# Performance work log

Measured on AMD Instinct MI355X. Metric: run time of the kernel, lower is better.

Reference implementation:

```python
import jax, jax.numpy as jnp
import numpy as np


def setup_inputs() -> dict:
    key = jax.random.key(0)
    k1, k2 = jax.random.split(key)
    # [batch, seq, in_features] activations
    x = jax.random.normal(k1, (4, 4096, 2048), dtype=jnp.float32)
    # fp32 master weight [out_features, in_features]; quantized inside reference
    weight = jax.random.normal(k2, (2048, 2048), dtype=jnp.float32) * 0.02
    return {"x": x, "weight": weight}


def reference(x, weight):
    num_bits = 8
    Qn = -(2 ** (num_bits - 1))       # -128
    Qp = 2 ** (num_bits - 1) - 1      # 127

    # Per-row absmax int8 activation quantization (activation_quant)
    si = Qp / jnp.clip(jnp.max(jnp.abs(x), axis=-1, keepdims=True), 1e-5)  # [B,S,1]
    qx = jnp.clip(jnp.round(x * si), Qn, Qp)  # int8 values held in fp32 (exact)

    # Ternary weight quantization (weight_quant): sw scalar = 1/mean|W|
    sw = 1.0 / jnp.clip(jnp.mean(jnp.abs(weight)), 1e-5)
    qw = jnp.clip(jnp.round(weight * sw), -1.0, 1.0)  # {-1,0,1}

    acc = jnp.einsum("bsk,nk->bsn", qx, qw)  # [B,S,out]

    # post_quant_process: dequantize by si and sw, cast to half
    out = ((acc / si) / sw).astype(jnp.float16)
    return out
```

## Files before the change

### kernel.cpp

```cpp
#include <hip/hip_runtime.h>

#define K_DIM 2048
#define N_DIM 2048
#define M_DIM 16384

typedef int v4i __attribute__((ext_vector_type(4)));


__device__ __forceinline__ void lds16(const void* g, void* l) {
    __builtin_amdgcn_global_load_lds(
        (const __attribute__((address_space(1))) unsigned int*)g,
        (__attribute__((address_space(3))) unsigned int*)l,
        16, 0, 0);
}

__global__ __launch_bounds__(256) void k_wsum(const float* __restrict__ w,
                                              double* __restrict__ wsum) {
    int tid = blockIdx.x * 256 + threadIdx.x;
    int stride = gridDim.x * 256;
    const float4* w4 = (const float4*)w;
    double s = 0.0;
    for (int i = tid; i < (N_DIM * K_DIM / 4); i += stride) {
        float4 v = w4[i];
        s += (double)fabsf(v.x);
        s += (double)fabsf(v.y);
        s += (double)fabsf(v.z);
        s += (double)fabsf(v.w);
    }
#pragma unroll
    for (int off = 32; off; off >>= 1) s += __shfl_xor(s, off, 64);
    __shared__ double part[4];
    int lane = threadIdx.x & 63, wv = threadIdx.x >> 6;
    if (lane == 0) part[wv] = s;
    __syncthreads();
    if (threadIdx.x == 0) atomicAdd(wsum, part[0] + part[1] + part[2] + part[3]);
}

__global__ __launch_bounds__(256) void k_quant_w(const float* __restrict__ w,
                                                 signed char* __restrict__ qw,
                                                 const double* __restrict__ wsum,
                                                 float* __restrict__ invsw_out) {
    float mean = (float)(*wsum * (1.0 / (double)(N_DIM * K_DIM)));
    float meanc = fmaxf(mean, 1e-5f);
    float sw = 1.0f / meanc;
    int tid = blockIdx.x * 256 + threadIdx.x;
    float4 v = ((const float4*)w)[tid];
    int q0 = (int)fminf(fmaxf(rintf(v.x * sw), -1.f), 1.f);
    int q1 = (int)fminf(fmaxf(rintf(v.y * sw), -1.f), 1.f);
    int q2 = (int)fminf(fmaxf(rintf(v.z * sw), -1.f), 1.f);
    int q3 = (int)fminf(fmaxf(rintf(v.w * sw), -1.f), 1.f);
    ((int*)qw)[tid] = (q0 & 255) | ((q1 & 255) << 8) | ((q2 & 255) << 16) | ((q3 & 255) << 24);
    if (tid == 0) *invsw_out = meanc;
}

__global__ __launch_bounds__(256) void k_quant_x(const float* __restrict__ x,
                                                 signed char* __restrict__ qx,
                                                 float* __restrict__ si_out) {
    int row = blockIdx.x * 4 + (threadIdx.x >> 6);
    int lane = threadIdx.x & 63;
    const float4* xr = (const float4*)(x + (size_t)row * K_DIM);
    float4 v[8];
    float mx = 0.f;
#pragma unroll
    for (int c = 0; c < 8; c++) {
        v[c] = xr[c * 64 + lane];
        mx = fmaxf(mx, fmaxf(fmaxf(fabsf(v[c].x), fabsf(v[c].y)),
                             fmaxf(fabsf(v[c].z), fabsf(v[c].w))));
    }
#pragma unroll
    for (int off = 32; off; off >>= 1) mx = fmaxf(mx, __shfl_xor(mx, off, 64));
    float si = 127.0f / fmaxf(mx, 1e-5f);
    if (lane == 0) si_out[row] = si;
    int* qr = (int*)(qx + (size_t)row * K_DIM);
#pragma unroll
    for (int c = 0; c < 8; c++) {
        int q0 = (int)fminf(fmaxf(rintf(v[c].x * si), -128.f), 127.f);
        int q1 = (int)fminf(fmaxf(rintf(v[c].y * si), -128.f), 127.f);
        int q2 = (int)fminf(fmaxf(rintf(v[c].z * si), -128.f), 127.f);
        int q3 = (int)fminf(fmaxf(rintf(v[c].w * si), -128.f), 127.f);
        qr[c * 64 + lane] = (q0 & 255) | ((q1 & 255) << 8) | ((q2 & 255) << 16) | ((q3 & 255) << 24);
    }
}

__global__ __launch_bounds__(256) void k_gemm(const signed char* __restrict__ qx,
                                              const signed char* __restrict__ qw,
                                              const float* __restrict__ si,
                                              const float* __restrict__ invsw_p,
                                              float* __restrict__ out) {
    __shared__ __align__(16) signed char As[128 * 64];
    __shared__ __align__(16) signed char Bs[128 * 64];
    const int t = threadIdx.x;
    const int lane = t & 63, wv = t >> 6;
    const int wr = wv >> 1, wc = wv & 1;
    const int lr = lane & 15, lq = lane >> 4;
    const int bm = blockIdx.y, bn = blockIdx.x;

    const int sRow = t >> 2;
    const int sCol = (t & 3) << 4;
    const signed char* aB0 = qx + (size_t)(bm * 128 + sRow) * K_DIM + sCol;
    const signed char* aB1 = aB0 + (size_t)64 * K_DIM;
    const signed char* bB0 = qw + (size_t)(bn * 128 + sRow) * K_DIM + sCol;
    const signed char* bB1 = bB0 + (size_t)64 * K_DIM;
    const int t16 = t << 4;

    v4i acc[4][4] = {};

    for (int k0 = 0; k0 < K_DIM; k0 += 64) {
        lds16(aB0 + k0, (signed char*)As + t16);
        lds16(aB1 + k0, (signed char*)As + 4096 + t16);
        lds16(bB0 + k0, (signed char*)Bs + t16);
        lds16(bB1 + k0, (signed char*)Bs + 4096 + t16);
        __syncthreads();

        v4i af[4], bf[4];
#pragma unroll
        for (int mt = 0; mt < 4; mt++)
            af[mt] = *(const v4i*)(As + ((wr * 64 + mt * 16 + lr) * 64 + lq * 16));
#pragma unroll
        for (int nt = 0; nt < 4; nt++)
            bf[nt] = *(const v4i*)(Bs + ((wc * 64 + nt * 16 + lr) * 64 + lq * 16));
#pragma unroll
        for (int mt = 0; mt < 4; mt++)
#pragma unroll
            for (int nt = 0; nt < 4; nt++)
                acc[mt][nt] = __builtin_amdgcn_mfma_i32_16x16x64_i8(af[mt], bf[nt], acc[mt][nt], 0, 0, 0);
        __syncthreads();
    }

    float invsw = *invsw_p;
#pragma unroll
    for (int mt = 0; mt < 4; mt++) {
        int rowb = bm * 128 + wr * 64 + mt * 16 + lq * 4;
        float sc[4];
#pragma unroll
        for (int r = 0; r < 4; r++) sc[r] = invsw / si[rowb + r];
#pragma unroll
        for (int nt = 0; nt < 4; nt++) {
            int col = bn * 128 + wc * 64 + nt * 16 + lr;
#pragma unroll
            for (int r = 0; r < 4; r++) {
                float vv = (float)acc[mt][nt][r] * sc[r];
                out[(size_t)(rowb + r) * N_DIM + col] = (float)(_Float16)vv;
            }
        }
    }
}

extern "C" void kernel_launch(void* const* d_in, const int* in_sizes, int n_in,
                              void* d_out, int out_size, void* d_ws, size_t ws_size,
                              hipStream_t stream) {
    const float* x = (const float*)d_in[0];
    const float* w = (const float*)d_in[1];
    float* out = (float*)d_out;
    char* ws = (char*)d_ws;

    double* wsum = (double*)ws;
    float* invsw = (float*)(ws + 8);
    float* si = (float*)(ws + 256);
    signed char* qw = (signed char*)(ws + 256 + 65536);
    signed char* qx = qw + (size_t)N_DIM * K_DIM;

    hipMemsetAsync(wsum, 0, 8, stream);
    k_wsum<<<1024, 256, 0, stream>>>(w, wsum);
    k_quant_w<<<4096, 256, 0, stream>>>(w, qw, wsum, invsw);
    k_quant_x<<<4096, 256, 0, stream>>>(x, qx, si);
    k_gemm<<<dim3(N_DIM / 128, M_DIM / 128), 256, 0, stream>>>(qx, qw, si, invsw, out);
}
```

Before: 336.3 us.

## Use 32x32x32 int8 MFMA with 256x128 tiles and deterministic weight-sum reduction

```diff
diff --git a/kernel.cpp b/kernel.cpp
--- a/kernel.cpp
+++ b/kernel.cpp
@@ -5,6 +5,7 @@
 #define M_DIM 16384
 
 typedef int v4i __attribute__((ext_vector_type(4)));
+typedef int v16i __attribute__((ext_vector_type(16)));
 
 
 __device__ __forceinline__ void lds16(const void* g, void* l) {
@@ -15,7 +16,7 @@
 }
 
 __global__ __launch_bounds__(256) void k_wsum(const float* __restrict__ w,
-                                              double* __restrict__ wsum) {
+                                              double* __restrict__ part) {
     int tid = blockIdx.x * 256 + threadIdx.x;
     int stride = gridDim.x * 256;
     const float4* w4 = (const float4*)w;
@@ -29,20 +30,33 @@
     }
 #pragma unroll
     for (int off = 32; off; off >>= 1) s += __shfl_xor(s, off, 64);
-    __shared__ double part[4];
+    __shared__ double sp[4];
     int lane = threadIdx.x & 63, wv = threadIdx.x >> 6;
-    if (lane == 0) part[wv] = s;
+    if (lane == 0) sp[wv] = s;
     __syncthreads();
-    if (threadIdx.x == 0) atomicAdd(wsum, part[0] + part[1] + part[2] + part[3]);
+    if (threadIdx.x == 0) part[blockIdx.x] = sp[0] + sp[1] + sp[2] + sp[3];
+}
+
+__global__ __launch_bounds__(256) void k_wred(const double* __restrict__ part,
+                                              float* __restrict__ invsw_out) {
+    double s = part[threadIdx.x];
+#pragma unroll
+    for (int off = 32; off; off >>= 1) s += __shfl_xor(s, off, 64);
+    __shared__ double sp[4];
+    int lane = threadIdx.x & 63, wv = threadIdx.x >> 6;
+    if (lane == 0) sp[wv] = s;
+    __syncthreads();
+    if (threadIdx.x == 0) {
+        double total = sp[0] + sp[1] + sp[2] + sp[3];
+        float mean = (float)(total * (1.0 / (double)(N_DIM * K_DIM)));
+        *invsw_out = fmaxf(mean, 1e-5f);
+    }
 }
 
 __global__ __launch_bounds__(256) void k_quant_w(const float* __restrict__ w,
                                                  signed char* __restrict__ qw,
-                                                 const double* __restrict__ wsum,
-                                                 float* __restrict__ invsw_out) {
-    float mean = (float)(*wsum * (1.0 / (double)(N_DIM * K_DIM)));
-    float meanc = fmaxf(mean, 1e-5f);
-    float sw = 1.0f / meanc;
+                                                 const float* __restrict__ invsw_p) {
+    float sw = 1.0f / (*invsw_p);
     int tid = blockIdx.x * 256 + threadIdx.x;
     float4 v = ((const float4*)w)[tid];
     int q0 = (int)fminf(fmaxf(rintf(v.x * sw), -1.f), 1.f);
@@ -50,7 +64,6 @@
     int q2 = (int)fminf(fmaxf(rintf(v.z * sw), -1.f), 1.f);
     int q3 = (int)fminf(fmaxf(rintf(v.w * sw), -1.f), 1.f);
     ((int*)qw)[tid] = (q0 & 255) | ((q1 & 255) << 8) | ((q2 & 255) << 16) | ((q3 & 255) << 24);
-    if (tid == 0) *invsw_out = meanc;
 }
 
 __global__ __launch_bounds__(256) void k_quant_x(const float* __restrict__ x,
@@ -82,65 +95,68 @@
     }
 }
 
-__global__ __launch_bounds__(256) void k_gemm(const signed char* __restrict__ qx,
-                                              const signed char* __restrict__ qw,
-                                              const float* __restrict__ si,
-                                              const float* __restrict__ invsw_p,
-                                              float* __restrict__ out) {
-    __shared__ __align__(16) signed char As[128 * 64];
-    __shared__ __align__(16) signed char Bs[128 * 64];
+__global__ __launch_bounds__(256, 2) void k_gemm(const signed char* __restrict__ qx,
+                                                 const signed char* __restrict__ qw,
+                                                 const float* __restrict__ si,
+                                                 const float* __restrict__ invsw_p,
+                                                 float* __restrict__ out) {
+    __shared__ __align__(16) signed char As[16384];
+    __shared__ __align__(16) signed char Bs[8192];
     const int t = threadIdx.x;
     const int lane = t & 63, wv = t >> 6;
     const int wr = wv >> 1, wc = wv & 1;
-    const int lr = lane & 15, lq = lane >> 4;
-    const int bm = blockIdx.y, bn = blockIdx.x;
+    const int l31 = lane & 31, lh = lane >> 5;
+    const int bn = blockIdx.x, bm = blockIdx.y;
 
-    const int sRow = t >> 2;
-    const int sCol = (t & 3) << 4;
-    const signed char* aB0 = qx + (size_t)(bm * 128 + sRow) * K_DIM + sCol;
-    const signed char* aB1 = aB0 + (size_t)64 * K_DIM;
-    const signed char* bB0 = qw + (size_t)(bn * 128 + sRow) * K_DIM + sCol;
-    const signed char* bB1 = bB0 + (size_t)64 * K_DIM;
+    const signed char* aG = qx + (size_t)(bm * 256 + t) * K_DIM;
+    const signed char* bG = qw + (size_t)(bn * 128 + (t & 127)) * K_DIM + ((t >> 7) << 4);
     const int t16 = t << 4;
 
-    v4i acc[4][4] = {};
+    v16i acc[4][2] = {};
 
     for (int k0 = 0; k0 < K_DIM; k0 += 64) {
-        lds16(aB0 + k0, (signed char*)As + t16);
-        lds16(aB1 + k0, (signed char*)As + 4096 + t16);
-        lds16(bB0 + k0, (signed char*)Bs + t16);
-        lds16(bB1 + k0, (signed char*)Bs + 4096 + t16);
+        lds16(aG + k0,      As + t16);
+        lds16(aG + k0 + 16, As + 4096 + t16);
+        lds16(aG + k0 + 32, As + 8192 + t16);
+        lds16(aG + k0 + 48, As + 12288 + t16);
+        lds16(bG + k0,      Bs + t16);
+        lds16(bG + k0 + 32, Bs + 4096 + t16);
         __syncthreads();
 
-        v4i af[4], bf[4];
 #pragma unroll
-        for (int mt = 0; mt < 4; mt++)
-            af[mt] = *(const v4i*)(As + ((wr * 64 + mt * 16 + lr) * 64 + lq * 16));
+        for (int ks = 0; ks < 2; ks++) {
+            v4i af[4], bf[2];
 #pragma unroll
-        for (int nt = 0; nt < 4; nt++)
-            bf[nt] = *(const v4i*)(Bs + ((wc * 64 + nt * 16 + lr) * 64 + lq * 16));
+            for (int mt = 0; mt < 4; mt++)
+                af[mt] = *(const v4i*)(As + (((ks * 2 + lh) * 256 + wr * 128 + mt * 32 + l31) << 4));
 #pragma unroll
-        for (int mt = 0; mt < 4; mt++)
+            for (int nt = 0; nt < 2; nt++)
+                bf[nt] = *(const v4i*)(Bs + (((ks * 2 + lh) * 128 + wc * 64 + nt * 32 + l31) << 4));
 #pragma unroll
-            for (int nt = 0; nt < 4; nt++)
-                acc[mt][nt] = __builtin_amdgcn_mfma_i32_16x16x64_i8(af[mt], bf[nt], acc[mt][nt], 0, 0, 0);
+            for (int mt = 0; mt < 4; mt++)
+#pragma unroll
+                for (int nt = 0; nt < 2; nt++)
+                    acc[mt][nt] = __builtin_amdgcn_mfma_i32_32x32x32_i8(af[mt], bf[nt], acc[mt][nt], 0, 0, 0);
+        }
         __syncthreads();
     }
 
     float invsw = *invsw_p;
 #pragma unroll
     for (int mt = 0; mt < 4; mt++) {
-        int rowb = bm * 128 + wr * 64 + mt * 16 + lq * 4;
-        float sc[4];
+        int rowb = bm * 256 + wr * 128 + mt * 32 + (lh << 2);
+        float sc[16];
 #pragma unroll
-        for (int r = 0; r < 4; r++) sc[r] = invsw / si[rowb + r];
+        for (int r = 0; r < 16; r++)
+            sc[r] = invsw / si[rowb + (r & 3) + ((r >> 2) << 3)];
 #pragma unroll
-        for (int nt = 0; nt < 4; nt++) {
-            int col = bn * 128 + wc * 64 + nt * 16 + lr;
+        for (int nt = 0; nt < 2; nt++) {
+            int col = bn * 128 + wc * 64 + nt * 32 + l31;
 #pragma unroll
-            for (int r = 0; r < 4; r++) {
+            for (int r = 0; r < 16; r++) {
+                int row = rowb + (r & 3) + ((r >> 2) << 3);
                 float vv = (float)acc[mt][nt][r] * sc[r];
-                out[(size_t)(rowb + r) * N_DIM + col] = (float)(_Float16)vv;
+                out[(size_t)row * N_DIM + col] = (float)(_Float16)vv;
             }
         }
     }
@@ -154,15 +170,15 @@
     float* out = (float*)d_out;
     char* ws = (char*)d_ws;
 
-    double* wsum = (double*)ws;
-    float* invsw = (float*)(ws + 8);
-    float* si = (float*)(ws + 256);
-    signed char* qw = (signed char*)(ws + 256 + 65536);
+    double* part = (double*)ws;
+    float* invsw = (float*)(ws + 2048);
+    float* si = (float*)(ws + 4096);
+    signed char* qw = (signed char*)(ws + 4096 + 65536);
     signed char* qx = qw + (size_t)N_DIM * K_DIM;
 
-    hipMemsetAsync(wsum, 0, 8, stream);
-    k_wsum<<<1024, 256, 0, stream>>>(w, wsum);
-    k_quant_w<<<4096, 256, 0, stream>>>(w, qw, wsum, invsw);
+    k_wsum<<<256, 256, 0, stream>>>(w, part);
+    k_wred<<<1, 256, 0, stream>>>(part, invsw);
     k_quant_x<<<4096, 256, 0, stream>>>(x, qx, si);
-    k_gemm<<<dim3(N_DIM / 128, M_DIM / 128), 256, 0, stream>>>(qx, qw, si, invsw, out);
+    k_quant_w<<<4096, 256, 0, stream>>>(w, qw, invsw);
+    k_gemm<<<dim3(N_DIM / 128, M_DIM / 256), 256, 0, stream>>>(qx, qw, si, invsw, out);
 }
```

New measurement: 373.6 us. 1.11x slower.
